# Performance work log

Measured on AMD Instinct MI355X. Metric: run time of the kernel, lower is better.

The kernel has to match this reference:

```python
import jax, jax.numpy as jnp
import numpy as np
from jax import lax

B, S, D, T = 64, 256, 1024, 60
HIST = 20  # last-20 window of attn / decoder-state history


def setup_inputs() -> dict:
    key = jax.random.key(0)
    ks = jax.random.split(key, 8)
    e_outputs = jax.random.normal(ks[0], (B, S, D), jnp.float32)
    queries = jax.random.normal(ks[1], (B, T, D), jnp.float32)
    # attention weights over source frames: rows sum to 1
    attns = jax.nn.softmax(jax.random.normal(ks[2], (B, T, S), jnp.float32), axis=-1)
    g = 0.02
    Wr = jax.random.normal(ks[3], (D, 1), jnp.float32) * g
    br = jnp.zeros((1,), jnp.float32)
    Wa = jax.random.normal(ks[4], (D, 1), jnp.float32) * g
    ba = jnp.zeros((1,), jnp.float32)
    Wq = jax.random.normal(ks[5], (D, D), jnp.float32) / np.sqrt(D)
    Wn = jax.random.normal(ks[6], (2 * D, 1), jnp.float32) * g
    bn = jnp.zeros((1,), jnp.float32)
    return {"e_outputs": e_outputs, "queries": queries, "attns": attns,
            "Wr": Wr, "br": br, "Wa": Wa, "ba": ba, "Wq": Wq, "Wn": Wn, "bn": bn}


def reference(e_outputs, queries, attns, Wr, br, Wa, ba, Wq, Wn, bn):
    Bn, Sn, Dn = e_outputs.shape
    # decay1[i] = (i+1)/20 ; decay2[i] = 1-(i+1)/50, zero-padded past 50 frames
    decay1 = (jnp.arange(HIST, dtype=jnp.float32) + 1.0) / 20.0
    idx = jnp.arange(Sn, dtype=jnp.float32)
    add0 = jnp.where(idx < 50, 1.0 - (idx + 1.0) / 50.0, 0.0)
    add_state0 = add0[None, :, None]                       # [1,S,1]
    mem0 = e_outputs * add_state0                          # [B,S,D]
    abuf0 = jnp.zeros((HIST, Bn, Sn), e_outputs.dtype)
    qbuf0 = jnp.zeros((HIST, Bn, Dn), e_outputs.dtype)

    def step(carry, x):
        mem, add_state, abuf, qbuf, i = carry
        attn_i, q_i = x                                    # [B,S], [B,D]
        # read: selected frame before memory update
        sel = jnp.einsum('bs,bsd->bd', attn_i, mem)
        # roll history buffers (newest at slot HIST-1)
        abuf = jnp.concatenate([abuf[1:], attn_i[None]], axis=0)
        qbuf = jnp.concatenate([qbuf[1:], q_i[None]], axis=0)
        k = jnp.minimum(i + 1, HIST)
        valid = jnp.arange(HIST) >= (HIST - k)
        temp = jax.nn.softmax(jnp.where(valid, decay1, -jnp.inf))
        attn_w = jnp.einsum('t,tbs->bs', temp, abuf)       # decayed attn sum
        query_s = jnp.einsum('t,tbd->bd', temp, qbuf)      # decayed query sum
        remove_prob = jax.nn.sigmoid(q_i @ Wr + br)[:, :, None]   # [B,1,1]
        add_prob = jax.nn.sigmoid(q_i @ Wa + ba)[:, :, None]      # [B,1,1]
        sim = jax.nn.sigmoid(jnp.einsum('bsd,bd->bs', mem, query_s @ Wq))[..., None]
        mem = mem * (1.0 - remove_prob * attn_w[..., None] * sim)
        last_ctx = jnp.einsum('bs,bsd->bd', attn_w, e_outputs)[:, None, :]
        cat = jnp.concatenate([e_outputs, jnp.broadcast_to(last_ctx, e_outputs.shape)], axis=-1)
        nxt = jax.nn.sigmoid(cat @ Wn + bn)                # [B,S,1]
        mem = mem + e_outputs * (1.0 - add_state) * (add_prob * nxt)
        add_state = add_state + (1.0 - add_state) * (add_prob * nxt)
        return (mem, add_state, abuf, qbuf, i + 1), sel

    init = (mem0, jnp.broadcast_to(add_state0, (Bn, Sn, 1)), abuf0, qbuf0, jnp.int32(0))
    xs = (attns.transpose(1, 0, 2), queries.transpose(1, 0, 2))
    _, sels = lax.scan(step, init, xs)
    return sels.transpose(1, 0, 2)                         # [B,T,D]
```

## Files before the change

kernel.cpp:

```cpp
#include <hip/hip_runtime.h>
#include <math.h>


#define Bn 64
#define Sn 256
#define Dn 1024
#define Tn 60
#define HISTn 20
#define LDK 72
#define K05 1.0512710963760241f
#define EINV 0.36787944117144233f

typedef __bf16 bf16x8 __attribute__((ext_vector_type(8)));
typedef float f32x4 __attribute__((ext_vector_type(4)));
typedef unsigned short us8 __attribute__((ext_vector_type(8)));

__device__ __forceinline__ unsigned short f2bf(float f){
  unsigned int x; __builtin_memcpy(&x,&f,4);
  unsigned int lsb = (x >> 16) & 1u;
  x += 0x7fffu + lsb;
  return (unsigned short)(x >> 16);
}
__device__ __forceinline__ float sigmoidf_(float x){ return 1.0f/(1.0f+expf(-x)); }

__global__ __launch_bounds__(256) void conv_qw(
    const float* __restrict__ Q, const float* __restrict__ Wr,
    const float* __restrict__ br, const float* __restrict__ Wa,
    const float* __restrict__ ba, const float* __restrict__ Wq,
    float* __restrict__ rp, float* __restrict__ ap,
    unsigned short* __restrict__ Qbf, unsigned short* __restrict__ WT)
{
  int tid = threadIdx.x;
  if (blockIdx.x < Bn*Tn){
    int row = blockIdx.x;
    float4 x = ((const float4*)(Q + (size_t)row*Dn))[tid];
    float4 a = ((const float4*)Wr)[tid];
    float4 b = ((const float4*)Wa)[tid];
    unsigned short o[4] = {f2bf(x.x), f2bf(x.y), f2bf(x.z), f2bf(x.w)};
    *(uint2*)&Qbf[(size_t)row*Dn + tid*4] = *(uint2*)o;
    float s1 = x.x*a.x + x.y*a.y + x.z*a.z + x.w*a.w;
    float s2 = x.x*b.x + x.y*b.y + x.z*b.z + x.w*b.w;
    for (int off = 32; off; off >>= 1){
      s1 += __shfl_down(s1, off, 64);
      s2 += __shfl_down(s2, off, 64);
    }
    __shared__ float r1[4], r2[4];
    int lane = tid & 63, wv = tid >> 6;
    if (lane == 0){ r1[wv] = s1; r2[wv] = s2; }
    __syncthreads();
    if (tid == 0){
      rp[row] = sigmoidf_(r1[0]+r1[1]+r1[2]+r1[3] + br[0]);
      ap[row] = sigmoidf_(r2[0]+r2[1]+r2[2]+r2[3] + ba[0]);
    }
  } else {
    __shared__ __align__(16) unsigned short Tt[64][LDK];
    int t = blockIdx.x - Bn*Tn;
    int n0 = (t >> 4)*64, k0 = (t & 15)*64;
    int kl = tid >> 4, nl4 = (tid & 15)*4;
    #pragma unroll
    for (int it = 0; it < 4; it++){
      int k = kl + it*16;
      float4 v = *(const float4*)&Wq[(size_t)(k0+k)*Dn + n0 + nl4];
      Tt[nl4+0][k] = f2bf(v.x); Tt[nl4+1][k] = f2bf(v.y);
      Tt[nl4+2][k] = f2bf(v.z); Tt[nl4+3][k] = f2bf(v.w);
    }
    __syncthreads();
    int nr = tid >> 2, kg = (tid & 3)*16;
    *(us8*)&WT[(size_t)(n0+nr)*Dn + k0+kg]   = *(us8*)&Tt[nr][kg];
    *(us8*)&WT[(size_t)(n0+nr)*Dn + k0+kg+8] = *(us8*)&Tt[nr][kg+8];
  }
}

__global__ __launch_bounds__(64) void conv_e(
    const float* __restrict__ E, const float* __restrict__ Wn,
    unsigned short* __restrict__ Ebf,
    float* __restrict__ eW1, float* __restrict__ eW2)
{
  int row = blockIdx.x, t = threadIdx.x;
  const float* er = E + (size_t)row*Dn;
  unsigned short* ebr = Ebf + (size_t)row*Dn;
  float d1 = 0.f, d2 = 0.f;
  #pragma unroll
  for (int c = 0; c < 4; c++){
    int idx = c*64 + t;
    float4 v = ((const float4*)er)[idx];
    float4 w1 = ((const float4*)Wn)[idx];
    float4 w2 = ((const float4*)(Wn + Dn))[idx];
    unsigned short o[4] = {f2bf(v.x), f2bf(v.y), f2bf(v.z), f2bf(v.w)};
    ((uint2*)ebr)[idx] = *(uint2*)o;
    d1 += v.x*w1.x + v.y*w1.y + v.z*w1.z + v.w*w1.w;
    d2 += v.x*w2.x + v.y*w2.y + v.z*w2.z + v.w*w2.w;
  }
  #pragma unroll
  for (int off = 32; off; off >>= 1){
    d1 += __shfl_down(d1, off, 64);
    d2 += __shfl_down(d2, off, 64);
  }
  if (t == 0){ eW1[row] = d1; eW2[row] = d2; }
}

__global__ __launch_bounds__(256) void gemm_qw(
    const unsigned short* __restrict__ Qbf,
    const unsigned short* __restrict__ WT,
    unsigned short* __restrict__ QWbf)
{
  __shared__ __align__(16) unsigned short As[64][LDK], Bs[64][LDK];
  int m0 = blockIdx.x*64, n0 = blockIdx.y*64;
  int tid = threadIdx.x, lane = tid & 63, wave = tid >> 6;
  int quad = lane >> 4, l16 = lane & 15;
  f32x4 acc[4];
  #pragma unroll
  for (int nt=0;nt<4;nt++)
    #pragma unroll
    for (int r=0;r<4;r++) acc[nt][r]=0.f;
  int sr = tid >> 2, sk = (tid & 3)*16;
  for (int k0 = 0; k0 < Dn; k0 += 64){
    *(us8*)&As[sr][sk]   = *(const us8*)&Qbf[(size_t)(m0+sr)*Dn + k0+sk];
    *(us8*)&As[sr][sk+8] = *(const us8*)&Qbf[(size_t)(m0+sr)*Dn + k0+sk+8];
    *(us8*)&Bs[sr][sk]   = *(const us8*)&WT[(size_t)(n0+sr)*Dn + k0+sk];
    *(us8*)&Bs[sr][sk+8] = *(const us8*)&WT[(size_t)(n0+sr)*Dn + k0+sk+8];
    __syncthreads();
    #pragma unroll
    for (int kk = 0; kk < 64; kk += 32){
      bf16x8 a = *(const bf16x8*)&As[wave*16 + l16][kk + quad*8];
      #pragma unroll
      for (int nt=0;nt<4;nt++){
        bf16x8 bb = *(const bf16x8*)&Bs[nt*16 + l16][kk + quad*8];
        acc[nt] = __builtin_amdgcn_mfma_f32_16x16x32_bf16(a, bb, acc[nt], 0, 0, 0);
      }
    }
    __syncthreads();
  }
  #pragma unroll
  for (int nt=0;nt<4;nt++)
    #pragma unroll
    for (int r=0;r<4;r++){
      int m = m0 + wave*16 + quad*4 + r;
      int n = n0 + nt*16 + l16;
      QWbf[(size_t)m*Dn + n] = f2bf(acc[nt][r]);
    }
}

__global__ __launch_bounds__(256) void gemm_g(
    const unsigned short* __restrict__ QWbf,
    const unsigned short* __restrict__ Ebf,
    float* __restrict__ G)
{
  __shared__ __align__(16) unsigned short As[64][LDK], Bs[32][LDK];
  int b = blockIdx.x, n0 = blockIdx.y*32;
  int tid = threadIdx.x, lane = tid & 63, wave = tid >> 6;
  int quad = lane >> 4, l16 = lane & 15;
  f32x4 acc[2];
  #pragma unroll
  for (int nt=0;nt<2;nt++)
    #pragma unroll
    for (int r=0;r<4;r++) acc[nt][r]=0.f;
  int sr = tid >> 2, sk = (tid & 3)*16;
  int brw = tid >> 3, bk = (tid & 7)*8;
  for (int k0 = 0; k0 < Dn; k0 += 64){
    if (sr < Tn){
      *(us8*)&As[sr][sk]   = *(const us8*)&QWbf[((size_t)(b*Tn + sr))*Dn + k0+sk];
      *(us8*)&As[sr][sk+8] = *(const us8*)&QWbf[((size_t)(b*Tn + sr))*Dn + k0+sk+8];
    } else {
      us8 z = (us8)0;
      *(us8*)&As[sr][sk] = z; *(us8*)&As[sr][sk+8] = z;
    }
    *(us8*)&Bs[brw][bk] = *(const us8*)&Ebf[((size_t)(b*Sn + n0 + brw))*Dn + k0 + bk];
    __syncthreads();
    #pragma unroll
    for (int kk = 0; kk < 64; kk += 32){
      bf16x8 a = *(const bf16x8*)&As[wave*16 + l16][kk + quad*8];
      #pragma unroll
      for (int nt=0;nt<2;nt++){
        bf16x8 bb = *(const bf16x8*)&Bs[nt*16 + l16][kk + quad*8];
        acc[nt] = __builtin_amdgcn_mfma_f32_16x16x32_bf16(a, bb, acc[nt], 0, 0, 0);
      }
    }
    __syncthreads();
  }
  #pragma unroll
  for (int nt=0;nt<2;nt++)
    #pragma unroll
    for (int r=0;r<4;r++){
      int t = wave*16 + quad*4 + r;
      int s = n0 + nt*16 + l16;
      if (t < Tn) G[((size_t)(b*Tn + t))*Sn + s] = acc[nt][r];
    }
}

__global__ __launch_bounds__(256) void kR_lc(
    const float* __restrict__ At,
    const float* __restrict__ eW2,
    float* __restrict__ lc)
{
  int b = blockIdx.x, tid = threadIdx.x;
  int lane = tid & 63, wv = tid >> 6;
  __shared__ float Rsh[Tn];
  float4 e2v = ((const float4*)(eW2 + (size_t)b*Sn))[lane];
  const float* at_b = At + (size_t)b*Tn*Sn;
  #pragma unroll
  for (int w = 0; w < 15; w++){
    int j = wv + w*4;
    float4 a4 = ((const float4*)(at_b + (size_t)j*Sn))[lane];
    float v = a4.x*e2v.x + a4.y*e2v.y + a4.z*e2v.z + a4.w*e2v.w;
    #pragma unroll
    for (int off = 32; off; off >>= 1) v += __shfl_down(v, off, 64);
    if (lane == 0) Rsh[j] = v;
  }
  __syncthreads();
  if (tid < Tn){
    int i = tid;
    int j0 = (i - HISTn + 1 > 0) ? i - HISTn + 1 : 0;
    float num = 0.f, den = 0.f;
    float wj = 1.f;
    for (int j = 0; j <= i; j++){
      wj *= K05;
      if (j >= j0){ num += wj * Rsh[j]; den += wj; }
    }
    lc[b*Tn + i] = num / den;
  }
}

__global__ __launch_bounds__(64) void scan_m(
    const float* __restrict__ At,
    const float* __restrict__ G,
    const float* __restrict__ rp,
    const float* __restrict__ ap,
    const float* __restrict__ eW1,
    const float* __restrict__ lc,
    const float* __restrict__ bnp,
    unsigned short* __restrict__ Pbf)
{
  int b = blockIdx.x, s0 = blockIdx.y * 64;
  int t = threadIdx.x;
  __shared__ __align__(16) float AtL[Tn][64], GL[Tn][64];
  __shared__ float lcs[Tn], rps[Tn], aps[Tn];
  const float* at_b = At + (size_t)b*Tn*Sn + s0;
  const float* g_b  = G  + (size_t)b*Tn*Sn + s0;
  #pragma unroll
  for (int r0 = 0; r0 < Tn; r0 += 4){
    int r = r0 + (t >> 4), c4 = (t & 15)*4;
    float4 av = *(const float4*)&at_b[(size_t)r*Sn + c4];
    float4 gv = *(const float4*)&g_b[(size_t)r*Sn + c4];
    *(float4*)&AtL[r][c4] = av;
    *(float4*)&GL[r][c4]  = gv;
  }
  if (t < Tn){
    lcs[t] = lc[b*Tn + t];
    rps[t] = rp[b*Tn + t];
    aps[t] = ap[b*Tn + t];
  }
  __syncthreads();
  int s = s0 + t;
  float M = (s < 50) ? (1.0f - (s+1)/50.0f) : 0.0f;
  float A = M;
  float bnv = bnp[0];
  float e1 = eW1[b*Sn + s];
  unsigned short* P_b = Pbf + (size_t)b*Tn*Sn + s;
  float num_a = 0.f, num_q = 0.f, den = 0.f, wi = 1.f;
  #pragma unroll
  for (int i = 0; i < Tn; i++){
    wi *= K05;
    float a_new = AtL[i][t];
    float g_new = GL[i][t];
    num_a += wi * a_new;
    num_q += wi * g_new;
    den   += wi;
    if (i >= HISTn){
      float wo = wi * EINV;
      num_a -= wo * AtL[i-HISTn][t];
      num_q -= wo * GL[i-HISTn][t];
      den   -= wo;
    }
    float inv = 1.0f / den;
    float aw = num_a * inv;
    float qd = num_q * inv;
    P_b[(size_t)i*Sn] = f2bf(a_new * M);
    float sim = sigmoidf_(M * qd);
    float nxt = sigmoidf_(e1 + lcs[i] + bnv);
    M = M * (1.0f - rps[i] * aw * sim);
    float g = (1.0f - A) * aps[i] * nxt;
    M += g; A += g;
  }
}

__global__ __launch_bounds__(256) void gemm_sels(
    const unsigned short* __restrict__ Pbf,
    const unsigned short* __restrict__ Ebf,
    float* __restrict__ out)
{
  __shared__ __align__(16) unsigned short As[64][LDK], Bs[64][LDK];
  int b = blockIdx.x, n0 = blockIdx.y*64;
  int tid = threadIdx.x, lane = tid & 63, wave = tid >> 6;
  int quad = lane >> 4, l16 = lane & 15;
  f32x4 acc[4];
  #pragma unroll
  for (int nt=0;nt<4;nt++)
    #pragma unroll
    for (int r=0;r<4;r++) acc[nt][r]=0.f;
  int sr = tid >> 2, sk = (tid & 3)*16;
  for (int k0 = 0; k0 < Sn; k0 += 64){
    if (sr < Tn){
      *(us8*)&As[sr][sk]   = *(const us8*)&Pbf[((size_t)(b*Tn + sr))*Sn + k0+sk];
      *(us8*)&As[sr][sk+8] = *(const us8*)&Pbf[((size_t)(b*Tn + sr))*Sn + k0+sk+8];
    } else {
      us8 z = (us8)0;
      *(us8*)&As[sr][sk] = z; *(us8*)&As[sr][sk+8] = z;
    }
    {
      const unsigned short* ep = &Ebf[((size_t)(b*Sn + k0 + sr))*Dn + n0 + sk];
      us8 e0 = *(const us8*)ep;
      us8 e1 = *(const us8*)(ep + 8);
      #pragma unroll
      for (int j=0;j<8;j++){
        Bs[sk+j][sr]   = e0[j];
        Bs[sk+8+j][sr] = e1[j];
      }
    }
    __syncthreads();
    #pragma unroll
    for (int kk = 0; kk < 64; kk += 32){
      bf16x8 a = *(const bf16x8*)&As[wave*16 + l16][kk + quad*8];
      #pragma unroll
      for (int nt=0;nt<4;nt++){
        bf16x8 bb = *(const bf16x8*)&Bs[nt*16 + l16][kk + quad*8];
        acc[nt] = __builtin_amdgcn_mfma_f32_16x16x32_bf16(a, bb, acc[nt], 0, 0, 0);
      }
    }
    __syncthreads();
  }
  #pragma unroll
  for (int nt=0;nt<4;nt++)
    #pragma unroll
    for (int r=0;r<4;r++){
      int t = wave*16 + quad*4 + r;
      int d = n0 + nt*16 + l16;
      if (t < Tn) out[((size_t)(b*Tn + t))*Dn + d] = acc[nt][r];
    }
}

extern "C" void kernel_launch(void* const* d_in, const int* in_sizes, int n_in,
                              void* d_out, int out_size, void* d_ws, size_t ws_size,
                              hipStream_t stream)
{
  const float* E  = (const float*)d_in[0];
  const float* Q  = (const float*)d_in[1];
  const float* At = (const float*)d_in[2];
  const float* Wr = (const float*)d_in[3];
  const float* br = (const float*)d_in[4];
  const float* Wa = (const float*)d_in[5];
  const float* ba = (const float*)d_in[6];
  const float* Wq = (const float*)d_in[7];
  const float* Wn = (const float*)d_in[8];
  const float* bnp= (const float*)d_in[9];

  char* ws = (char*)d_ws;
  float* rp  = (float*)ws; ws += (size_t)Bn*Tn*4;
  float* ap  = (float*)ws; ws += (size_t)Bn*Tn*4;
  float* eW1 = (float*)ws; ws += (size_t)Bn*Sn*4;
  float* eW2 = (float*)ws; ws += (size_t)Bn*Sn*4;
  float* lcb = (float*)ws; ws += (size_t)Bn*Tn*4;
  unsigned short* Qbf  = (unsigned short*)ws; ws += (size_t)Bn*Tn*Dn*2;
  unsigned short* WT   = (unsigned short*)ws; ws += (size_t)Dn*Dn*2;
  unsigned short* QWbf = (unsigned short*)ws; ws += (size_t)Bn*Tn*Dn*2;
  unsigned short* Ebf  = (unsigned short*)ws; ws += (size_t)Bn*Sn*Dn*2;
  float* G = (float*)ws; ws += (size_t)Bn*Tn*Sn*4;
  unsigned short* Pbf = (unsigned short*)ws; ws += (size_t)Bn*Tn*Sn*2;

  conv_qw<<<Bn*Tn + 256, 256, 0, stream>>>(Q, Wr, br, Wa, ba, Wq, rp, ap, Qbf, WT);
  conv_e<<<Bn*Sn, 64, 0, stream>>>(E, Wn, Ebf, eW1, eW2);
  gemm_qw<<<dim3(Bn*Tn/64, Dn/64), 256, 0, stream>>>(Qbf, WT, QWbf);
  gemm_g<<<dim3(Bn, Sn/32), 256, 0, stream>>>(QWbf, Ebf, G);
  kR_lc<<<Bn, 256, 0, stream>>>(At, eW2, lcb);
  scan_m<<<dim3(Bn, Sn/64), 64, 0, stream>>>(At, G, rp, ap, eW1, lcb, bnp, Pbf);
  gemm_sels<<<dim3(Bn, Dn/64), 256, 0, stream>>>(Pbf, Ebf, (float*)d_out);
}
```

Measured before the change: 210.5 us.

## Fuse prep kernels, merge G GEMM into scan, use direct-to-LDS loads

Merges the Q/W conversion and E conversion into one launch, folds the last-context reduction into the Q·Wq GEMM launch as extra blocks, and computes the G tile inside the scan kernel so G never goes to global memory. The Q·Wq GEMM now stages tiles with global_load_lds and an XOR-swizzled LDS layout. This cuts launch count and a global round trip for G. In exchange, the scan runs serially on one wave while the other three sit idle, and the larger LDS footprint may lower occupancy.

```diff
diff --git a/kernel.cpp b/kernel.cpp
--- a/kernel.cpp
+++ b/kernel.cpp
@@ -15,6 +15,13 @@
 typedef float f32x4 __attribute__((ext_vector_type(4)));
 typedef unsigned short us8 __attribute__((ext_vector_type(8)));
 
+typedef const __attribute__((address_space(1))) unsigned int* gas_u32p;
+typedef __attribute__((address_space(3))) unsigned int* las_u32p;
+
+__device__ __forceinline__ void gl16(const unsigned short* g, unsigned short* l){
+  __builtin_amdgcn_global_load_lds((gas_u32p)g, (las_u32p)l, 16, 0, 0);
+}
+
 __device__ __forceinline__ unsigned short f2bf(float f){
   unsigned int x; __builtin_memcpy(&x,&f,4);
   unsigned int lsb = (x >> 16) & 1u;
@@ -23,16 +30,20 @@
 }
 __device__ __forceinline__ float sigmoidf_(float x){ return 1.0f/(1.0f+expf(-x)); }
 
-__global__ __launch_bounds__(256) void conv_qw(
+__global__ __launch_bounds__(256) void conv_fused(
     const float* __restrict__ Q, const float* __restrict__ Wr,
     const float* __restrict__ br, const float* __restrict__ Wa,
     const float* __restrict__ ba, const float* __restrict__ Wq,
+    const float* __restrict__ E, const float* __restrict__ Wn,
     float* __restrict__ rp, float* __restrict__ ap,
-    unsigned short* __restrict__ Qbf, unsigned short* __restrict__ WT)
+    unsigned short* __restrict__ Qbf, unsigned short* __restrict__ WT,
+    unsigned short* __restrict__ Ebf,
+    float* __restrict__ eW1, float* __restrict__ eW2)
 {
   int tid = threadIdx.x;
-  if (blockIdx.x < Bn*Tn){
-    int row = blockIdx.x;
+  int bx = blockIdx.x;
+  if (bx < Bn*Tn){
+    int row = bx;
     float4 x = ((const float4*)(Q + (size_t)row*Dn))[tid];
     float4 a = ((const float4*)Wr)[tid];
     float4 b = ((const float4*)Wa)[tid];
@@ -52,9 +63,9 @@
       rp[row] = sigmoidf_(r1[0]+r1[1]+r1[2]+r1[3] + br[0]);
       ap[row] = sigmoidf_(r2[0]+r2[1]+r2[2]+r2[3] + ba[0]);
     }
-  } else {
+  } else if (bx < Bn*Tn + 256){
     __shared__ __align__(16) unsigned short Tt[64][LDK];
-    int t = blockIdx.x - Bn*Tn;
+    int t = bx - Bn*Tn;
     int n0 = (t >> 4)*64, k0 = (t & 15)*64;
     int kl = tid >> 4, nl4 = (tid & 15)*4;
     #pragma unroll
@@ -68,162 +79,124 @@
     int nr = tid >> 2, kg = (tid & 3)*16;
     *(us8*)&WT[(size_t)(n0+nr)*Dn + k0+kg]   = *(us8*)&Tt[nr][kg];
     *(us8*)&WT[(size_t)(n0+nr)*Dn + k0+kg+8] = *(us8*)&Tt[nr][kg+8];
-  }
-}
-
-__global__ __launch_bounds__(64) void conv_e(
-    const float* __restrict__ E, const float* __restrict__ Wn,
-    unsigned short* __restrict__ Ebf,
-    float* __restrict__ eW1, float* __restrict__ eW2)
-{
-  int row = blockIdx.x, t = threadIdx.x;
-  const float* er = E + (size_t)row*Dn;
-  unsigned short* ebr = Ebf + (size_t)row*Dn;
-  float d1 = 0.f, d2 = 0.f;
-  #pragma unroll
-  for (int c = 0; c < 4; c++){
-    int idx = c*64 + t;
-    float4 v = ((const float4*)er)[idx];
-    float4 w1 = ((const float4*)Wn)[idx];
-    float4 w2 = ((const float4*)(Wn + Dn))[idx];
-    unsigned short o[4] = {f2bf(v.x), f2bf(v.y), f2bf(v.z), f2bf(v.w)};
-    ((uint2*)ebr)[idx] = *(uint2*)o;
-    d1 += v.x*w1.x + v.y*w1.y + v.z*w1.z + v.w*w1.w;
-    d2 += v.x*w2.x + v.y*w2.y + v.z*w2.z + v.w*w2.w;
-  }
-  #pragma unroll
-  for (int off = 32; off; off >>= 1){
-    d1 += __shfl_down(d1, off, 64);
-    d2 += __shfl_down(d2, off, 64);
-  }
-  if (t == 0){ eW1[row] = d1; eW2[row] = d2; }
-}
-
-__global__ __launch_bounds__(256) void gemm_qw(
+  } else {
+    int row = (bx - (Bn*Tn + 256))*4 + (tid >> 6);
+    int lane = tid & 63;
+    const float* er = E + (size_t)row*Dn;
+    unsigned short* ebr = Ebf + (size_t)row*Dn;
+    float d1 = 0.f, d2 = 0.f;
+    #pragma unroll
+    for (int c = 0; c < 4; c++){
+      int idx = c*64 + lane;
+      float4 v = ((const float4*)er)[idx];
+      float4 w1 = ((const float4*)Wn)[idx];
+      float4 w2 = ((const float4*)(Wn + Dn))[idx];
+      unsigned short o[4] = {f2bf(v.x), f2bf(v.y), f2bf(v.z), f2bf(v.w)};
+      ((uint2*)ebr)[idx] = *(uint2*)o;
+      d1 += v.x*w1.x + v.y*w1.y + v.z*w1.z + v.w*w1.w;
+      d2 += v.x*w2.x + v.y*w2.y + v.z*w2.z + v.w*w2.w;
+    }
+    #pragma unroll
+    for (int off = 32; off; off >>= 1){
+      d1 += __shfl_down(d1, off, 64);
+      d2 += __shfl_down(d2, off, 64);
+    }
+    if (lane == 0){ eW1[row] = d1; eW2[row] = d2; }
+  }
+}
+
+__global__ __launch_bounds__(256) void gemm_qw_kr(
     const unsigned short* __restrict__ Qbf,
     const unsigned short* __restrict__ WT,
-    unsigned short* __restrict__ QWbf)
-{
-  __shared__ __align__(16) unsigned short As[64][LDK], Bs[64][LDK];
-  int m0 = blockIdx.x*64, n0 = blockIdx.y*64;
-  int tid = threadIdx.x, lane = tid & 63, wave = tid >> 6;
-  int quad = lane >> 4, l16 = lane & 15;
-  f32x4 acc[4];
-  #pragma unroll
-  for (int nt=0;nt<4;nt++)
-    #pragma unroll
-    for (int r=0;r<4;r++) acc[nt][r]=0.f;
-  int sr = tid >> 2, sk = (tid & 3)*16;
-  for (int k0 = 0; k0 < Dn; k0 += 64){
-    *(us8*)&As[sr][sk]   = *(const us8*)&Qbf[(size_t)(m0+sr)*Dn + k0+sk];
-    *(us8*)&As[sr][sk+8] = *(const us8*)&Qbf[(size_t)(m0+sr)*Dn + k0+sk+8];
-    *(us8*)&Bs[sr][sk]   = *(const us8*)&WT[(size_t)(n0+sr)*Dn + k0+sk];
-    *(us8*)&Bs[sr][sk+8] = *(const us8*)&WT[(size_t)(n0+sr)*Dn + k0+sk+8];
-    __syncthreads();
-    #pragma unroll
-    for (int kk = 0; kk < 64; kk += 32){
-      bf16x8 a = *(const bf16x8*)&As[wave*16 + l16][kk + quad*8];
-      #pragma unroll
-      for (int nt=0;nt<4;nt++){
-        bf16x8 bb = *(const bf16x8*)&Bs[nt*16 + l16][kk + quad*8];
-        acc[nt] = __builtin_amdgcn_mfma_f32_16x16x32_bf16(a, bb, acc[nt], 0, 0, 0);
-      }
-    }
-    __syncthreads();
-  }
-  #pragma unroll
-  for (int nt=0;nt<4;nt++)
-    #pragma unroll
-    for (int r=0;r<4;r++){
-      int m = m0 + wave*16 + quad*4 + r;
-      int n = n0 + nt*16 + l16;
-      QWbf[(size_t)m*Dn + n] = f2bf(acc[nt][r]);
-    }
-}
-
-__global__ __launch_bounds__(256) void gemm_g(
+    const float* __restrict__ At,
+    const float* __restrict__ eW2,
+    unsigned short* __restrict__ QWbf,
+    float* __restrict__ lc)
+{
+  int tid = threadIdx.x;
+  if (blockIdx.x < (Bn*Tn/64)*(Dn/64)){
+    __shared__ __align__(16) unsigned short As[64*64], Bs[64*64];
+    int bx = blockIdx.x;
+    int m0 = (bx >> 4) * 64, n0 = (bx & 15) * 64;
+    int lane = tid & 63, wave = tid >> 6;
+    int quad = lane >> 4, l16 = lane & 15;
+    f32x4 acc[4];
+    #pragma unroll
+    for (int nt=0;nt<4;nt++)
+      #pragma unroll
+      for (int r=0;r<4;r++) acc[nt][r]=0.f;
+    int c0 = wave*2;
+    int srow = c0*8 + (lane >> 3);
+    int scol = ((lane & 7) ^ (lane >> 3)) * 8;
+    const unsigned short* gA0 = Qbf + (size_t)(m0 + srow)*Dn + scol;
+    const unsigned short* gA1 = gA0 + 8*Dn;
+    const unsigned short* gB0 = WT  + (size_t)(n0 + srow)*Dn + scol;
+    const unsigned short* gB1 = gB0 + 8*Dn;
+    unsigned short* lA0 = &As[c0*512];
+    unsigned short* lA1 = &As[c0*512 + 512];
+    unsigned short* lB0 = &Bs[c0*512];
+    unsigned short* lB1 = &Bs[c0*512 + 512];
+    int mrow = wave*16 + l16;
+    for (int k0 = 0; k0 < Dn; k0 += 64){
+      gl16(gA0 + k0, lA0);
+      gl16(gA1 + k0, lA1);
+      gl16(gB0 + k0, lB0);
+      gl16(gB1 + k0, lB1);
+      __syncthreads();
+      #pragma unroll
+      for (int kk = 0; kk < 2; kk++){
+        bf16x8 a = *(const bf16x8*)&As[ mrow*64 + ((kk*32 + quad*8) ^ ((mrow&7)*8)) ];
+        #pragma unroll
+        for (int nt=0;nt<4;nt++){
+          int nrow = nt*16 + l16;
+          bf16x8 bb = *(const bf16x8*)&Bs[ nrow*64 + ((kk*32 + quad*8) ^ ((nrow&7)*8)) ];
+          acc[nt] = __builtin_amdgcn_mfma_f32_16x16x32_bf16(a, bb, acc[nt], 0, 0, 0);
+        }
+      }
+      __syncthreads();
+    }
+    #pragma unroll
+    for (int nt=0;nt<4;nt++)
+      #pragma unroll
+      for (int r=0;r<4;r++){
+        int m = m0 + wave*16 + quad*4 + r;
+        int n = n0 + nt*16 + l16;
+        QWbf[(size_t)m*Dn + n] = f2bf(acc[nt][r]);
+      }
+  } else {
+    int b = blockIdx.x - (Bn*Tn/64)*(Dn/64);
+    int lane = tid & 63, wv = tid >> 6;
+    __shared__ float Rsh[Tn];
+    float4 e2v = ((const float4*)(eW2 + (size_t)b*Sn))[lane];
+    const float* at_b = At + (size_t)b*Tn*Sn;
+    #pragma unroll
+    for (int w = 0; w < 15; w++){
+      int j = wv + w*4;
+      float4 a4 = ((const float4*)(at_b + (size_t)j*Sn))[lane];
+      float v = a4.x*e2v.x + a4.y*e2v.y + a4.z*e2v.z + a4.w*e2v.w;
+      #pragma unroll
+      for (int off = 32; off; off >>= 1) v += __shfl_down(v, off, 64);
+      if (lane == 0) Rsh[j] = v;
+    }
+    __syncthreads();
+    if (tid < Tn){
+      int i = tid;
+      int j0 = (i - HISTn + 1 > 0) ? i - HISTn + 1 : 0;
+      float num = 0.f, den = 0.f;
+      float wj = 1.f;
+      for (int j = 0; j <= i; j++){
+        wj *= K05;
+        if (j >= j0){ num += wj * Rsh[j]; den += wj; }
+      }
+      lc[b*Tn + i] = num / den;
+    }
+  }
+}
+
+__global__ __launch_bounds__(256) void g_scan(
     const unsigned short* __restrict__ QWbf,
     const unsigned short* __restrict__ Ebf,
-    float* __restrict__ G)
-{
-  __shared__ __align__(16) unsigned short As[64][LDK], Bs[32][LDK];
-  int b = blockIdx.x, n0 = blockIdx.y*32;
-  int tid = threadIdx.x, lane = tid & 63, wave = tid >> 6;
-  int quad = lane >> 4, l16 = lane & 15;
-  f32x4 acc[2];
-  #pragma unroll
-  for (int nt=0;nt<2;nt++)
-    #pragma unroll
-    for (int r=0;r<4;r++) acc[nt][r]=0.f;
-  int sr = tid >> 2, sk = (tid & 3)*16;
-  int brw = tid >> 3, bk = (tid & 7)*8;
-  for (int k0 = 0; k0 < Dn; k0 += 64){
-    if (sr < Tn){
-      *(us8*)&As[sr][sk]   = *(const us8*)&QWbf[((size_t)(b*Tn + sr))*Dn + k0+sk];
-      *(us8*)&As[sr][sk+8] = *(const us8*)&QWbf[((size_t)(b*Tn + sr))*Dn + k0+sk+8];
-    } else {
-      us8 z = (us8)0;
-      *(us8*)&As[sr][sk] = z; *(us8*)&As[sr][sk+8] = z;
-    }
-    *(us8*)&Bs[brw][bk] = *(const us8*)&Ebf[((size_t)(b*Sn + n0 + brw))*Dn + k0 + bk];
-    __syncthreads();
-    #pragma unroll
-    for (int kk = 0; kk < 64; kk += 32){
-      bf16x8 a = *(const bf16x8*)&As[wave*16 + l16][kk + quad*8];
-      #pragma unroll
-      for (int nt=0;nt<2;nt++){
-        bf16x8 bb = *(const bf16x8*)&Bs[nt*16 + l16][kk + quad*8];
-        acc[nt] = __builtin_amdgcn_mfma_f32_16x16x32_bf16(a, bb, acc[nt], 0, 0, 0);
-      }
-    }
-    __syncthreads();
-  }
-  #pragma unroll
-  for (int nt=0;nt<2;nt++)
-    #pragma unroll
-    for (int r=0;r<4;r++){
-      int t = wave*16 + quad*4 + r;
-      int s = n0 + nt*16 + l16;
-      if (t < Tn) G[((size_t)(b*Tn + t))*Sn + s] = acc[nt][r];
-    }
-}
-
-__global__ __launch_bounds__(256) void kR_lc(
     const float* __restrict__ At,
-    const float* __restrict__ eW2,
-    float* __restrict__ lc)
-{
-  int b = blockIdx.x, tid = threadIdx.x;
-  int lane = tid & 63, wv = tid >> 6;
-  __shared__ float Rsh[Tn];
-  float4 e2v = ((const float4*)(eW2 + (size_t)b*Sn))[lane];
-  const float* at_b = At + (size_t)b*Tn*Sn;
-  #pragma unroll
-  for (int w = 0; w < 15; w++){
-    int j = wv + w*4;
-    float4 a4 = ((const float4*)(at_b + (size_t)j*Sn))[lane];
-    float v = a4.x*e2v.x + a4.y*e2v.y + a4.z*e2v.z + a4.w*e2v.w;
-    #pragma unroll
-    for (int off = 32; off; off >>= 1) v += __shfl_down(v, off, 64);
-    if (lane == 0) Rsh[j] = v;
-  }
-  __syncthreads();
-  if (tid < Tn){
-    int i = tid;
-    int j0 = (i - HISTn + 1 > 0) ? i - HISTn + 1 : 0;
-    float num = 0.f, den = 0.f;
-    float wj = 1.f;
-    for (int j = 0; j <= i; j++){
-      wj *= K05;
-      if (j >= j0){ num += wj * Rsh[j]; den += wj; }
-    }
-    lc[b*Tn + i] = num / den;
-  }
-}
-
-__global__ __launch_bounds__(64) void scan_m(
-    const float* __restrict__ At,
-    const float* __restrict__ G,
     const float* __restrict__ rp,
     const float* __restrict__ ap,
     const float* __restrict__ eW1,
@@ -231,56 +204,99 @@
     const float* __restrict__ bnp,
     unsigned short* __restrict__ Pbf)
 {
-  int b = blockIdx.x, s0 = blockIdx.y * 64;
-  int t = threadIdx.x;
+  __shared__ __align__(16) unsigned short As[64][LDK], Bs[64][LDK];
   __shared__ __align__(16) float AtL[Tn][64], GL[Tn][64];
   __shared__ float lcs[Tn], rps[Tn], aps[Tn];
+  int b = blockIdx.x, s0 = blockIdx.y * 64;
+  int tid = threadIdx.x, lane = tid & 63, wave = tid >> 6;
+  int quad = lane >> 4, l16 = lane & 15;
+
   const float* at_b = At + (size_t)b*Tn*Sn + s0;
-  const float* g_b  = G  + (size_t)b*Tn*Sn + s0;
-  #pragma unroll
-  for (int r0 = 0; r0 < Tn; r0 += 4){
-    int r = r0 + (t >> 4), c4 = (t & 15)*4;
-    float4 av = *(const float4*)&at_b[(size_t)r*Sn + c4];
-    float4 gv = *(const float4*)&g_b[(size_t)r*Sn + c4];
-    *(float4*)&AtL[r][c4] = av;
-    *(float4*)&GL[r][c4]  = gv;
-  }
-  if (t < Tn){
-    lcs[t] = lc[b*Tn + t];
-    rps[t] = rp[b*Tn + t];
-    aps[t] = ap[b*Tn + t];
-  }
+  #pragma unroll
+  for (int it = 0; it < 4; it++){
+    int r = it*16 + (tid >> 4);
+    if (r < Tn){
+      int c4 = (tid & 15)*4;
+      *(float4*)&AtL[r][c4] = *(const float4*)&at_b[(size_t)r*Sn + c4];
+    }
+  }
+  if (tid < Tn){
+    lcs[tid] = lc[b*Tn + tid];
+    rps[tid] = rp[b*Tn + tid];
+    aps[tid] = ap[b*Tn + tid];
+  }
+
+  f32x4 acc[4];
+  #pragma unroll
+  for (int nt=0;nt<4;nt++)
+    #pragma unroll
+    for (int r=0;r<4;r++) acc[nt][r]=0.f;
+  int sr = tid >> 2, sk = (tid & 3)*16;
+  const unsigned short* aRow = QWbf + ((size_t)(b*Tn + sr))*Dn;
+  const unsigned short* bRow = Ebf  + ((size_t)(b*Sn + s0 + sr))*Dn;
+  for (int k0 = 0; k0 < Dn; k0 += 64){
+    if (sr < Tn){
+      *(us8*)&As[sr][sk]   = *(const us8*)&aRow[k0+sk];
+      *(us8*)&As[sr][sk+8] = *(const us8*)&aRow[k0+sk+8];
+    } else {
+      us8 z = (us8)0;
+      *(us8*)&As[sr][sk] = z; *(us8*)&As[sr][sk+8] = z;
+    }
+    *(us8*)&Bs[sr][sk]   = *(const us8*)&bRow[k0+sk];
+    *(us8*)&Bs[sr][sk+8] = *(const us8*)&bRow[k0+sk+8];
+    __syncthreads();
+    #pragma unroll
+    for (int kk = 0; kk < 64; kk += 32){
+      bf16x8 a = *(const bf16x8*)&As[wave*16 + l16][kk + quad*8];
+      #pragma unroll
+      for (int nt=0;nt<4;nt++){
+        bf16x8 bb = *(const bf16x8*)&Bs[nt*16 + l16][kk + quad*8];
+        acc[nt] = __builtin_amdgcn_mfma_f32_16x16x32_bf16(a, bb, acc[nt], 0, 0, 0);
+      }
+    }
+    __syncthreads();
+  }
+  #pragma unroll
+  for (int nt=0;nt<4;nt++)
+    #pragma unroll
+    for (int r=0;r<4;r++){
+      int t = wave*16 + quad*4 + r;
+      if (t < Tn) GL[t][nt*16 + l16] = acc[nt][r];
+    }
   __syncthreads();
-  int s = s0 + t;
-  float M = (s < 50) ? (1.0f - (s+1)/50.0f) : 0.0f;
-  float A = M;
-  float bnv = bnp[0];
-  float e1 = eW1[b*Sn + s];
-  unsigned short* P_b = Pbf + (size_t)b*Tn*Sn + s;
-  float num_a = 0.f, num_q = 0.f, den = 0.f, wi = 1.f;
-  #pragma unroll
-  for (int i = 0; i < Tn; i++){
-    wi *= K05;
-    float a_new = AtL[i][t];
-    float g_new = GL[i][t];
-    num_a += wi * a_new;
-    num_q += wi * g_new;
-    den   += wi;
-    if (i >= HISTn){
-      float wo = wi * EINV;
-      num_a -= wo * AtL[i-HISTn][t];
-      num_q -= wo * GL[i-HISTn][t];
-      den   -= wo;
-    }
-    float inv = 1.0f / den;
-    float aw = num_a * inv;
-    float qd = num_q * inv;
-    P_b[(size_t)i*Sn] = f2bf(a_new * M);
-    float sim = sigmoidf_(M * qd);
-    float nxt = sigmoidf_(e1 + lcs[i] + bnv);
-    M = M * (1.0f - rps[i] * aw * sim);
-    float g = (1.0f - A) * aps[i] * nxt;
-    M += g; A += g;
+
+  if (tid < 64){
+    int s = s0 + tid;
+    float M = (s < 50) ? (1.0f - (s+1)/50.0f) : 0.0f;
+    float A = M;
+    float bnv = bnp[0];
+    float e1 = eW1[b*Sn + s];
+    unsigned short* P_b = Pbf + (size_t)b*Tn*Sn + s;
+    float num_a = 0.f, num_q = 0.f, den = 0.f, wi = 1.f;
+    #pragma unroll
+    for (int i = 0; i < Tn; i++){
+      wi *= K05;
+      float a_new = AtL[i][tid];
+      float g_new = GL[i][tid];
+      num_a += wi * a_new;
+      num_q += wi * g_new;
+      den   += wi;
+      if (i >= HISTn){
+        float wo = wi * EINV;
+        num_a -= wo * AtL[i-HISTn][tid];
+        num_q -= wo * GL[i-HISTn][tid];
+        den   -= wo;
+      }
+      float inv = 1.0f / den;
+      float aw = num_a * inv;
+      float qd = num_q * inv;
+      P_b[(size_t)i*Sn] = f2bf(a_new * M);
+      float sim = sigmoidf_(M * qd);
+      float nxt = sigmoidf_(e1 + lcs[i] + bnv);
+      M = M * (1.0f - rps[i] * aw * sim);
+      float g = (1.0f - A) * aps[i] * nxt;
+      M += g; A += g;
+    }
   }
 }
 
@@ -364,14 +380,13 @@
   unsigned short* WT   = (unsigned short*)ws; ws += (size_t)Dn*Dn*2;
   unsigned short* QWbf = (unsigned short*)ws; ws += (size_t)Bn*Tn*Dn*2;
   unsigned short* Ebf  = (unsigned short*)ws; ws += (size_t)Bn*Sn*Dn*2;
-  float* G = (float*)ws; ws += (size_t)Bn*Tn*Sn*4;
   unsigned short* Pbf = (unsigned short*)ws; ws += (size_t)Bn*Tn*Sn*2;
 
-  conv_qw<<<Bn*Tn + 256, 256, 0, stream>>>(Q, Wr, br, Wa, ba, Wq, rp, ap, Qbf, WT);
-  conv_e<<<Bn*Sn, 64, 0, stream>>>(E, Wn, Ebf, eW1, eW2);
-  gemm_qw<<<dim3(Bn*Tn/64, Dn/64), 256, 0, stream>>>(Qbf, WT, QWbf);
-  gemm_g<<<dim3(Bn, Sn/32), 256, 0, stream>>>(QWbf, Ebf, G);
-  kR_lc<<<Bn, 256, 0, stream>>>(At, eW2, lcb);
-  scan_m<<<dim3(Bn, Sn/64), 64, 0, stream>>>(At, G, rp, ap, eW1, lcb, bnp, Pbf);
+  conv_fused<<<Bn*Tn + 256 + Bn*Sn/4, 256, 0, stream>>>(
+      Q, Wr, br, Wa, ba, Wq, E, Wn, rp, ap, Qbf, WT, Ebf, eW1, eW2);
+  gemm_qw_kr<<<(Bn*Tn/64)*(Dn/64) + Bn, 256, 0, stream>>>(
+      Qbf, WT, At, eW2, QWbf, lcb);
+  g_scan<<<dim3(Bn, Sn/64), 256, 0, stream>>>(
+      QWbf, Ebf, At, rp, ap, eW1, lcb, bnp, Pbf);
   gemm_sels<<<dim3(Bn, Dn/64), 256, 0, stream>>>(Pbf, Ebf, (float*)d_out);
 }
```

Result: faster. 193.3 us (-8.1%).
